# Kernel optimization log

Measured on AMD Instinct MI355X. Metric: run time of the kernel, lower is better.

## Reference

```python
import jax, jax.numpy as jnp
import numpy as np

N = 100000   # nodes
E = 600000   # edges
G = 64       # graphs in batch
H = 128      # hidden size
F_NODE = 2
F_EDGE = 7
RH = 500     # reghead size
NEG_SLOPE = 0.01
BN_EPS = 1e-5


def leaky(x):
    return jnp.where(x >= 0, x, NEG_SLOPE * x)


def gine_conv(x, src, dst, edge_attr, edge_W, edge_b, W1, b1, gamma, beta, W2, b2):
    # PyG GINEConv: message = ReLU(x_j + Lin(edge_attr)); sum-aggregate at dst;
    # out = nn((1+eps)*x + aggr) with eps=0; nn = Lin -> BN(train) -> LeakyReLU -> Lin -> LeakyReLU
    e = edge_attr @ edge_W.T + edge_b                 # [E, d_in]
    m = jax.nn.relu(x[src] + e)                       # gather + add + relu
    aggr = jax.ops.segment_sum(m, dst, num_segments=N)
    h = x + aggr
    h = h @ W1.T + b1                                 # [N, H]
    mu = jnp.mean(h, axis=0)
    var = jnp.var(h, axis=0)                          # biased, matches BN training
    h = gamma * (h - mu) * jax.lax.rsqrt(var + BN_EPS) + beta
    h = leaky(h)
    h = h @ W2.T + b2
    return leaky(h)


def setup_inputs() -> dict:
    key = jax.random.key(0)
    ks = jax.random.split(key, 24)

    def lin(k, out_d, in_d):
        s = 1.0 / np.sqrt(in_d)
        k1, k2 = jax.random.split(k)
        return (jax.random.uniform(k1, (out_d, in_d), jnp.float32, -s, s),
                jax.random.uniform(k2, (out_d,), jnp.float32, -s, s))

    x = jax.random.normal(ks[0], (N, F_NODE), jnp.float32)
    edge_index = jax.random.randint(ks[1], (2, E), 0, N, jnp.int32)
    batch = jnp.sort(jax.random.randint(ks[2], (N,), 0, G, jnp.int32))
    edge_attr = jax.random.normal(ks[3], (E, F_EDGE), jnp.float32)

    # layer 0 (in_dim = F_NODE)
    ew0, eb0 = lin(ks[4], F_NODE, F_EDGE)
    w10, b10 = lin(ks[5], H, F_NODE)
    g0, be0 = jnp.ones((H,), jnp.float32), jnp.zeros((H,), jnp.float32)
    w20, b20 = lin(ks[6], H, H)

    # 3 hidden layers, stacked (in_dim = H)
    L = 3
    ewS = jnp.stack([lin(ks[7 + i], H, F_EDGE)[0] for i in range(L)])
    ebS = jnp.stack([lin(jax.random.fold_in(ks[7 + i], 1), H, F_EDGE)[1] for i in range(L)])
    w1S = jnp.stack([lin(ks[10 + i], H, H)[0] for i in range(L)])
    b1S = jnp.stack([lin(jax.random.fold_in(ks[10 + i], 1), H, H)[1] for i in range(L)])
    gS = jnp.ones((L, H), jnp.float32)
    beS = jnp.zeros((L, H), jnp.float32)
    w2S = jnp.stack([lin(ks[13 + i], H, H)[0] for i in range(L)])
    b2S = jnp.stack([lin(jax.random.fold_in(ks[13 + i], 1), H, H)[1] for i in range(L)])

    wr, br = lin(ks[16], RH, H)
    we, be_ = lin(ks[17], 1, RH)

    return {"x": x, "edge_index": edge_index, "batch": batch, "edge_attr": edge_attr,
            "ew0": ew0, "eb0": eb0, "w10": w10, "b10": b10, "g0": g0, "be0": be0,
            "w20": w20, "b20": b20,
            "ewS": ewS, "ebS": ebS, "w1S": w1S, "b1S": b1S, "gS": gS, "beS": beS,
            "w2S": w2S, "b2S": b2S, "wr": wr, "br": br, "we": we, "be_": be_}


def reference(x, edge_index, batch, edge_attr,
              ew0, eb0, w10, b10, g0, be0, w20, b20,
              ewS, ebS, w1S, b1S, gS, beS, w2S, b2S,
              wr, br, we, be_):
    src, dst = edge_index[0], edge_index[1]
    h = gine_conv(x, src, dst, edge_attr, ew0, eb0, w10, b10, g0, be0, w20, b20)
    h = leaky(h)  # outer self.relu; dropout p=0 is identity
    for i in range(ewS.shape[0]):
        h = gine_conv(h, src, dst, edge_attr, ewS[i], ebS[i], w1S[i], b1S[i],
                      gS[i], beS[i], w2S[i], b2S[i])
        h = leaky(h)
    # global_mean_pool
    sums = jax.ops.segment_sum(h, batch, num_segments=G)
    cnt = jax.ops.segment_sum(jnp.ones((h.shape[0],), h.dtype), batch, num_segments=G)
    pooled = sums / jnp.maximum(cnt, 1.0)[:, None]
    # reghead_layers == 2
    r = leaky(pooled @ wr.T + br)
    return r @ we.T + be_
```

## Files before the change

kernel.cpp:

```cpp
#include <hip/hip_runtime.h>

#define NNODES 100000
#define NEDGES 600000
#define NGRAPH 64
#define HID 128
#define RHD 500
#define NB ((NNODES + 255) / 256)
#define EB ((NEDGES + 255) / 256)
#define GG ((NNODES + 63) / 64)

typedef __attribute__((ext_vector_type(8))) short short8;
typedef __attribute__((ext_vector_type(4))) float f32x4;

__device__ __forceinline__ float leaky1(float x) { return x >= 0.0f ? x : 0.01f * x; }

__device__ __forceinline__ void splitf(float a, unsigned short& h, unsigned short& l)
{
    unsigned u = __float_as_uint(a);
    unsigned r = (u + 0x7FFFu + ((u >> 16) & 1u)) & 0xFFFF0000u;
    h = (unsigned short)(r >> 16);
    float res = a - __uint_as_float(r);
    unsigned u2 = __float_as_uint(res);
    l = (unsigned short)((u2 + 0x7FFFu + ((u2 >> 16) & 1u)) >> 16);
}

__global__ __launch_bounds__(256) void hist_kernel(
    const int* __restrict__ ei, int* __restrict__ deg)
{
    int e = blockIdx.x * 256 + threadIdx.x;
    if (e < NEDGES) atomicAdd(&deg[ei[NEDGES + e]], 1);
}

__global__ __launch_bounds__(256) void scan_blk(
    const int* __restrict__ deg, int* __restrict__ incl, int* __restrict__ bsum)
{
    __shared__ int s[256];
    int t = threadIdx.x;
    int n = blockIdx.x * 256 + t;
    int v = (n < NNODES) ? deg[n] : 0;
    int x = v;
    s[t] = x;
    __syncthreads();
    for (int off = 1; off < 256; off <<= 1) {
        int y = (t >= off) ? s[t - off] : 0;
        __syncthreads();
        x += y; s[t] = x;
        __syncthreads();
    }
    if (n < NNODES) incl[n] = x;
    if (t == 255) bsum[blockIdx.x] = x;
}

__global__ __launch_bounds__(512) void scan_bsum(int* __restrict__ bsum, int nblk)
{
    __shared__ int s[512];
    int t = threadIdx.x;
    int v = (t < nblk) ? bsum[t] : 0;
    int x = v;
    s[t] = x;
    __syncthreads();
    for (int off = 1; off < 512; off <<= 1) {
        int y = (t >= off) ? s[t - off] : 0;
        __syncthreads();
        x += y; s[t] = x;
        __syncthreads();
    }
    if (t < nblk) bsum[t] = x - v;
}

__global__ __launch_bounds__(256) void finalize_rp(
    const int* __restrict__ deg, const int* __restrict__ bsum,
    int* __restrict__ rp, int* __restrict__ cursor)
{
    int n = blockIdx.x * 256 + threadIdx.x;
    if (n >= NNODES) return;
    int ig = rp[n] + bsum[blockIdx.x];
    int st = ig - deg[n];
    rp[n] = st;
    cursor[n] = st;
    if (n == NNODES - 1) rp[NNODES] = ig;
}

__global__ __launch_bounds__(256) void scatter_kernel(
    const int* __restrict__ ei, int* __restrict__ cursor, int* __restrict__ eid)
{
    int e = blockIdx.x * 256 + threadIdx.x;
    if (e >= NEDGES) return;
    int d = ei[NEDGES + e];
    int pos = atomicAdd(&cursor[d], 1);
    eid[pos] = e;
}

__global__ __launch_bounds__(256) void seg_sort(
    const int* __restrict__ rp, int* __restrict__ eid)
{
    int n = blockIdx.x * 256 + threadIdx.x;
    if (n >= NNODES) return;
    int beg = rp[n], end = rp[n + 1];
    for (int i = beg + 1; i < end; ++i) {
        int key = eid[i];
        int j = i - 1;
        while (j >= beg && eid[j] > key) { eid[j + 1] = eid[j]; --j; }
        eid[j + 1] = key;
    }
}

__global__ __launch_bounds__(256) void permute_kernel(
    const int* __restrict__ eid, const int* __restrict__ ei,
    const float* __restrict__ ea, int* __restrict__ srcp, float* __restrict__ eap)
{
    int p = blockIdx.x * 256 + threadIdx.x;
    if (p >= NEDGES) return;
    int id = eid[p];
    srcp[p] = ei[id];
    const float* s = ea + (size_t)id * 7;
    float* d = eap + (size_t)p * 7;
#pragma unroll
    for (int k = 0; k < 7; ++k) d[k] = s[k];
}

__global__ __launch_bounds__(256) void wsplit_all(
    const float* __restrict__ w20, const float* __restrict__ w1S,
    const float* __restrict__ w2S,
    unsigned short* __restrict__ wh, unsigned short* __restrict__ wl)
{
    int i = blockIdx.x * 256 + threadIdx.x;
    int m = i >> 14;
    int off = i & 16383;
    const float* src;
    if (m == 0) src = w20;
    else if (m <= 3) src = w1S + (size_t)(m - 1) * 16384;
    else src = w2S + (size_t)(m - 4) * 16384;
    unsigned short h, l;
    splitf(src[off], h, l);
    wh[i] = h;
    wl[i] = l;
}

__global__ __launch_bounds__(256) void aggregate0_kernel(
    const float* __restrict__ x, const int* __restrict__ rp,
    const int* __restrict__ srcp, const float* __restrict__ eap,
    const float* __restrict__ ew, const float* __restrict__ eb,
    float* __restrict__ aggr2)
{
    int n = blockIdx.x * 256 + threadIdx.x;
    if (n >= NNODES) return;
    float w0[7], w1[7];
#pragma unroll
    for (int k = 0; k < 7; ++k) { w0[k] = ew[k]; w1[k] = ew[7 + k]; }
    float e0b = eb[0], e1b = eb[1];
    float a0 = x[n * 2 + 0], a1 = x[n * 2 + 1];
    int beg = rp[n], end = rp[n + 1];
    for (int e = beg; e < end; ++e) {
        int s = srcp[e];
        const float* ap = eap + (size_t)e * 7;
        float t0 = e0b, t1 = e1b;
#pragma unroll
        for (int k = 0; k < 7; ++k) {
            float av = ap[k];
            t0 = fmaf(av, w0[k], t0);
            t1 = fmaf(av, w1[k], t1);
        }
        a0 += fmaxf(x[s * 2 + 0] + t0, 0.0f);
        a1 += fmaxf(x[s * 2 + 1] + t1, 0.0f);
    }
    aggr2[n * 2 + 0] = a0;
    aggr2[n * 2 + 1] = a1;
}

__global__ __launch_bounds__(256) void aggregate_kernel(
    const float* __restrict__ hin, const int* __restrict__ rp,
    const int* __restrict__ srcp, const float* __restrict__ eap,
    const float* __restrict__ ew, const float* __restrict__ eb,
    unsigned short* __restrict__ Ahi, unsigned short* __restrict__ Alo)
{
    int lane = threadIdx.x & 63;
    int w = threadIdx.x >> 6;
    int nbase = blockIdx.x * 32 + w * 8;
    float ew0[7], ew1[7];
#pragma unroll
    for (int k = 0; k < 7; ++k) {
        ew0[k] = ew[lane * 7 + k];
        ew1[k] = ew[(lane + 64) * 7 + k];
    }
    float eb0v = eb[lane], eb1v = eb[lane + 64];
    for (int n = nbase; n < nbase + 8; ++n) {
        float a0 = hin[(size_t)n * HID + lane];
        float a1 = hin[(size_t)n * HID + 64 + lane];
        int beg = rp[n], end = rp[n + 1];
        int e = beg;
        for (; e + 4 <= end; e += 4) {
            int s0 = srcp[e], s1 = srcp[e + 1], s2 = srcp[e + 2], s3 = srcp[e + 3];
            const float* ap = eap + (size_t)e * 7;
            float x00 = hin[(size_t)s0 * HID + lane];
            float x01 = hin[(size_t)s0 * HID + 64 + lane];
            float x10 = hin[(size_t)s1 * HID + lane];
            float x11 = hin[(size_t)s1 * HID + 64 + lane];
            float x20 = hin[(size_t)s2 * HID + lane];
            float x21 = hin[(size_t)s2 * HID + 64 + lane];
            float x30 = hin[(size_t)s3 * HID + lane];
            float x31 = hin[(size_t)s3 * HID + 64 + lane];
            float t00 = eb0v, t01 = eb1v, t10 = eb0v, t11 = eb1v;
            float t20 = eb0v, t21 = eb1v, t30 = eb0v, t31 = eb1v;
#pragma unroll
            for (int k = 0; k < 7; ++k) {
                float av0 = ap[k], av1 = ap[7 + k], av2 = ap[14 + k], av3 = ap[21 + k];
                t00 = fmaf(av0, ew0[k], t00); t01 = fmaf(av0, ew1[k], t01);
                t10 = fmaf(av1, ew0[k], t10); t11 = fmaf(av1, ew1[k], t11);
                t20 = fmaf(av2, ew0[k], t20); t21 = fmaf(av2, ew1[k], t21);
                t30 = fmaf(av3, ew0[k], t30); t31 = fmaf(av3, ew1[k], t31);
            }
            a0 += fmaxf(x00 + t00, 0.0f);
            a1 += fmaxf(x01 + t01, 0.0f);
            a0 += fmaxf(x10 + t10, 0.0f);
            a1 += fmaxf(x11 + t11, 0.0f);
            a0 += fmaxf(x20 + t20, 0.0f);
            a1 += fmaxf(x21 + t21, 0.0f);
            a0 += fmaxf(x30 + t30, 0.0f);
            a1 += fmaxf(x31 + t31, 0.0f);
        }
        for (; e < end; ++e) {
            int s = srcp[e];
            const float* ap = eap + (size_t)e * 7;
            float t0 = eb0v, t1 = eb1v;
#pragma unroll
            for (int k = 0; k < 7; ++k) {
                float av = ap[k];
                t0 = fmaf(av, ew0[k], t0);
                t1 = fmaf(av, ew1[k], t1);
            }
            float x0 = hin[(size_t)s * HID + lane];
            float x1 = hin[(size_t)s * HID + 64 + lane];
            a0 += fmaxf(x0 + t0, 0.0f);
            a1 += fmaxf(x1 + t1, 0.0f);
        }
        unsigned short h0, l0, h1v, l1v;
        splitf(a0, h0, l0);
        splitf(a1, h1v, l1v);
        size_t rb = (size_t)n * HID;
        Ahi[rb + lane] = h0;
        Ahi[rb + 64 + lane] = h1v;
        Alo[rb + lane] = l0;
        Alo[rb + 64 + lane] = l1v;
    }
}

__global__ __launch_bounds__(256) void gemm1_l0_kernel(
    const float* __restrict__ aggr2,
    const float* __restrict__ w1, const float* __restrict__ b1,
    float* __restrict__ h1)
{
    int n = blockIdx.x * 256 + threadIdx.x;
    if (n >= NNODES) return;
    float x0 = aggr2[n * 2 + 0];
    float x1 = aggr2[n * 2 + 1];
    float4* out4 = (float4*)(h1 + (size_t)n * HID);
    for (int j = 0; j < HID; j += 4) {
        float4 o;
        o.x = fmaf(x1, w1[(j + 0) * 2 + 1], fmaf(x0, w1[(j + 0) * 2 + 0], b1[j + 0]));
        o.y = fmaf(x1, w1[(j + 1) * 2 + 1], fmaf(x0, w1[(j + 1) * 2 + 0], b1[j + 1]));
        o.z = fmaf(x1, w1[(j + 2) * 2 + 1], fmaf(x0, w1[(j + 2) * 2 + 0], b1[j + 2]));
        o.w = fmaf(x1, w1[(j + 3) * 2 + 1], fmaf(x0, w1[(j + 3) * 2 + 0], b1[j + 3]));
        out4[j >> 2] = o;
    }
}

__global__ __launch_bounds__(256) void bn_stats_part(
    const float* __restrict__ h1, float* __restrict__ part)
{
    __shared__ float ls[HID], lq[HID];
    int c = threadIdx.x & 127;
    int half = threadIdx.x >> 7;
    int base = blockIdx.x * 256;
    int end = base + 256; if (end > NNODES) end = NNODES;
    float s = 0.0f, q = 0.0f;
    for (int r = base + half; r < end; r += 2) {
        float v = h1[(size_t)r * HID + c];
        s += v;
        q = fmaf(v, v, q);
    }
    if (half) { ls[c] = s; lq[c] = q; }
    __syncthreads();
    if (!half) {
        s += ls[c]; q += lq[c];
        part[(size_t)blockIdx.x * 256 + c] = s;
        part[(size_t)blockIdx.x * 256 + 128 + c] = q;
    }
}

__global__ __launch_bounds__(64) void bn_finalize(
    const float* __restrict__ part, int nblk,
    const float* __restrict__ gamma, const float* __restrict__ beta,
    float* __restrict__ scsh)
{
    int c = blockIdx.x;
    int lane = threadIdx.x;
    float s = 0.0f, q = 0.0f;
    for (int i = lane; i < nblk; i += 64) {
        s += part[(size_t)i * 256 + c];
        q += part[(size_t)i * 256 + 128 + c];
    }
#pragma unroll
    for (int off = 32; off >= 1; off >>= 1) {
        s += __shfl_down(s, off);
        q += __shfl_down(q, off);
    }
    if (lane == 0) {
        const float invN = 1.0f / (float)NNODES;
        float mu = s * invN;
        float var = fmaf(-mu, mu, q * invN);
        float iv = rsqrtf(var + 1e-5f);
        float sc = gamma[c] * iv;
        scsh[c] = sc;
        scsh[HID + c] = beta[c] - mu * sc;
    }
}

__global__ __launch_bounds__(256) void gemm1_direct(
    const unsigned short* __restrict__ Ahi, const unsigned short* __restrict__ Alo,
    const unsigned short* __restrict__ wh, const unsigned short* __restrict__ wl,
    const float* __restrict__ b1, float* __restrict__ h1,
    float* __restrict__ part)
{
    __shared__ float red[1024];
    const int t = threadIdx.x;
    const int lane = t & 63;
    const int wv = t >> 6;
    const int cl = lane & 15, g = lane >> 4;
    const int mb = blockIdx.x * 64;
    const int colbase = wv * 32;

    const unsigned short* wb_h0 = wh + (size_t)(colbase + cl) * HID + g * 8;
    const unsigned short* wb_h1 = wb_h0 + 16 * HID;
    const unsigned short* wb_l0 = wl + (size_t)(colbase + cl) * HID + g * 8;
    const unsigned short* wb_l1 = wb_l0 + 16 * HID;

    int arow[4];
#pragma unroll
    for (int rt = 0; rt < 4; ++rt) {
        int r = mb + rt * 16 + cl;
        arow[rt] = r < NNODES ? r : NNODES - 1;
    }

    f32x4 acc[4][2];
#pragma unroll
    for (int rt = 0; rt < 4; ++rt) {
        acc[rt][0] = (f32x4){0.f, 0.f, 0.f, 0.f};
        acc[rt][1] = (f32x4){0.f, 0.f, 0.f, 0.f};
    }

#pragma unroll
    for (int ks = 0; ks < 4; ++ks) {
        short8 bh0 = *(const short8*)(wb_h0 + ks * 32);
        short8 bh1 = *(const short8*)(wb_h1 + ks * 32);
        short8 bl0 = *(const short8*)(wb_l0 + ks * 32);
        short8 bl1 = *(const short8*)(wb_l1 + ks * 32);
        int koff = ks * 32 + g * 8;
#pragma unroll
        for (int rt = 0; rt < 4; ++rt) {
            short8 ah = *(const short8*)(Ahi + (size_t)arow[rt] * HID + koff);
            short8 al = *(const short8*)(Alo + (size_t)arow[rt] * HID + koff);
            acc[rt][0] = __builtin_amdgcn_mfma_f32_16x16x32_bf16(ah, bh0, acc[rt][0], 0, 0, 0);
            acc[rt][1] = __builtin_amdgcn_mfma_f32_16x16x32_bf16(ah, bh1, acc[rt][1], 0, 0, 0);
            acc[rt][0] = __builtin_amdgcn_mfma_f32_16x16x32_bf16(al, bh0, acc[rt][0], 0, 0, 0);
            acc[rt][1] = __builtin_amdgcn_mfma_f32_16x16x32_bf16(al, bh1, acc[rt][1], 0, 0, 0);
            acc[rt][0] = __builtin_amdgcn_mfma_f32_16x16x32_bf16(ah, bl0, acc[rt][0], 0, 0, 0);
            acc[rt][1] = __builtin_amdgcn_mfma_f32_16x16x32_bf16(ah, bl1, acc[rt][1], 0, 0, 0);
        }
    }

    float bj0 = b1[colbase + cl];
    float bj1 = b1[colbase + 16 + cl];
    float s0 = 0.f, q0 = 0.f, s1 = 0.f, q1 = 0.f;
#pragma unroll
    for (int rt = 0; rt < 4; ++rt) {
        int rbase = mb + rt * 16 + g * 4;
#pragma unroll
        for (int r = 0; r < 4; ++r) {
            int grow = rbase + r;
            if (grow < NNODES) {
                float o0 = acc[rt][0][r] + bj0;
                float o1 = acc[rt][1][r] + bj1;
                h1[(size_t)grow * HID + colbase + cl] = o0;
                h1[(size_t)grow * HID + colbase + 16 + cl] = o1;
                s0 += o0; q0 = fmaf(o0, o0, q0);
                s1 += o1; q1 = fmaf(o1, o1, q1);
            }
        }
    }
    red[(colbase + cl) * 4 + g] = s0;
    red[(colbase + 16 + cl) * 4 + g] = s1;
    red[512 + (colbase + cl) * 4 + g] = q0;
    red[512 + (colbase + 16 + cl) * 4 + g] = q1;
    __syncthreads();
    {
        int stat = t >> 7, col = t & 127;
        const float* bp = red + stat * 512 + col * 4;
        part[(size_t)blockIdx.x * 256 + stat * 128 + col] = bp[0] + bp[1] + bp[2] + bp[3];
    }
}

template<int PRE, int POST>
__global__ __launch_bounds__(256) void gemm_mfma(
    const float* __restrict__ Ain, const float* __restrict__ scsh,
    const unsigned short* __restrict__ wh, const unsigned short* __restrict__ wl,
    const float* __restrict__ bias, float* __restrict__ Hout)
{
    __shared__ __align__(16) short lds[16384];
    const int t = threadIdx.x;
    const int mb = blockIdx.x * 64;

    const float4* sc4 = (const float4*)scsh;
    const float4* sh4 = (const float4*)(scsh + HID);

#pragma unroll
    for (int u = 0; u < 4; ++u) {
        int idx = u * 256 + t;
        int row = idx >> 4, sl = idx & 15;
        float4 v0 = make_float4(0.f, 0.f, 0.f, 0.f);
        float4 v1 = make_float4(0.f, 0.f, 0.f, 0.f);
        int gr = mb + row;
        if (gr < NNODES) {
            const float4* p = (const float4*)(Ain + (size_t)gr * HID + sl * 8);
            v0 = p[0]; v1 = p[1];
            if (PRE) {
                float4 c0 = sc4[sl * 2], c1 = sc4[sl * 2 + 1];
                float4 s0 = sh4[sl * 2], s1 = sh4[sl * 2 + 1];
                v0.x = leaky1(fmaf(v0.x, c0.x, s0.x));
                v0.y = leaky1(fmaf(v0.y, c0.y, s0.y));
                v0.z = leaky1(fmaf(v0.z, c0.z, s0.z));
                v0.w = leaky1(fmaf(v0.w, c0.w, s0.w));
                v1.x = leaky1(fmaf(v1.x, c1.x, s1.x));
                v1.y = leaky1(fmaf(v1.y, c1.y, s1.y));
                v1.z = leaky1(fmaf(v1.z, c1.z, s1.z));
                v1.w = leaky1(fmaf(v1.w, c1.w, s1.w));
            }
        }
        unsigned short h[8], l[8];
        splitf(v0.x, h[0], l[0]); splitf(v0.y, h[1], l[1]);
        splitf(v0.z, h[2], l[2]); splitf(v0.w, h[3], l[3]);
        splitf(v1.x, h[4], l[4]); splitf(v1.y, h[5], l[5]);
        splitf(v1.z, h[6], l[6]); splitf(v1.w, h[7], l[7]);
        short8 hv, lv;
#pragma unroll
        for (int e = 0; e < 8; ++e) { hv[e] = (short)h[e]; lv[e] = (short)l[e]; }
        int byt = row * 256 + ((sl ^ (row & 7)) << 4);
        *(short8*)((char*)lds + byt) = hv;
        *(short8*)((char*)lds + 16384 + byt) = lv;
    }
    __syncthreads();

    const int lane = t & 63;
    const int wv = t >> 6;
    const int cl = lane & 15, g = lane >> 4, x = lane & 7;
    const int colbase = wv * 32;

    int aoff[4];
#pragma unroll
    for (int ks = 0; ks < 4; ++ks)
        aoff[ks] = cl * 256 + (((ks * 4 + g) ^ x) << 4);

    const unsigned short* wb_h0 = wh + (size_t)(colbase + cl) * HID + g * 8;
    const unsigned short* wb_h1 = wb_h0 + 16 * HID;
    const unsigned short* wb_l0 = wl + (size_t)(colbase + cl) * HID + g * 8;
    const unsigned short* wb_l1 = wb_l0 + 16 * HID;

    f32x4 acc[4][2];
#pragma unroll
    for (int rt = 0; rt < 4; ++rt) {
        acc[rt][0] = (f32x4){0.f, 0.f, 0.f, 0.f};
        acc[rt][1] = (f32x4){0.f, 0.f, 0.f, 0.f};
    }

#pragma unroll
    for (int ks = 0; ks < 4; ++ks) {
        short8 bh0 = *(const short8*)(wb_h0 + ks * 32);
        short8 bh1 = *(const short8*)(wb_h1 + ks * 32);
        short8 bl0 = *(const short8*)(wb_l0 + ks * 32);
        short8 bl1 = *(const short8*)(wb_l1 + ks * 32);
#pragma unroll
        for (int rt = 0; rt < 4; ++rt) {
            short8 ah = *(const short8*)((const char*)lds + (rt * 4096) + aoff[ks]);
            short8 al = *(const short8*)((const char*)lds + (16384 + rt * 4096) + aoff[ks]);
            acc[rt][0] = __builtin_amdgcn_mfma_f32_16x16x32_bf16(ah, bh0, acc[rt][0], 0, 0, 0);
            acc[rt][1] = __builtin_amdgcn_mfma_f32_16x16x32_bf16(ah, bh1, acc[rt][1], 0, 0, 0);
            acc[rt][0] = __builtin_amdgcn_mfma_f32_16x16x32_bf16(al, bh0, acc[rt][0], 0, 0, 0);
            acc[rt][1] = __builtin_amdgcn_mfma_f32_16x16x32_bf16(al, bh1, acc[rt][1], 0, 0, 0);
            acc[rt][0] = __builtin_amdgcn_mfma_f32_16x16x32_bf16(ah, bl0, acc[rt][0], 0, 0, 0);
            acc[rt][1] = __builtin_amdgcn_mfma_f32_16x16x32_bf16(ah, bl1, acc[rt][1], 0, 0, 0);
        }
    }

    float bj0 = bias[colbase + cl];
    float bj1 = bias[colbase + 16 + cl];
#pragma unroll
    for (int rt = 0; rt < 4; ++rt) {
        int rbase = mb + rt * 16 + g * 4;
#pragma unroll
        for (int r = 0; r < 4; ++r) {
            int grow = rbase + r;
            if (grow < NNODES) {
                float o0 = acc[rt][0][r] + bj0;
                float o1 = acc[rt][1][r] + bj1;
                if (POST) { o0 = leaky1(leaky1(o0)); o1 = leaky1(leaky1(o1)); }
                Hout[(size_t)grow * HID + colbase + cl] = o0;
                Hout[(size_t)grow * HID + colbase + 16 + cl] = o1;
            }
        }
    }
}

__global__ __launch_bounds__(256) void pool_kernel(
    const float* __restrict__ h, const int* __restrict__ batch,
    float* __restrict__ sums, float* __restrict__ cnt)
{
    int c = threadIdx.x & 127;
    int half = threadIdx.x >> 7;
    int base = blockIdx.x * 128 + half * 64;
    if (base >= NNODES) return;
    int end = base + 64; if (end > NNODES) end = NNODES;
    int g = batch[base];
    float acc = 0.0f, k = 0.0f;
    for (int n = base; n < end; ++n) {
        int gn = batch[n];
        if (gn != g) {
            atomicAdd(&sums[g * HID + c], acc);
            if (c == 0) atomicAdd(&cnt[g], k);
            acc = 0.0f; k = 0.0f; g = gn;
        }
        acc += h[(size_t)n * HID + c];
        k += 1.0f;
    }
    atomicAdd(&sums[g * HID + c], acc);
    if (c == 0) atomicAdd(&cnt[g], k);
}

__global__ __launch_bounds__(512) void reghead_kernel(
    const float* __restrict__ sums, const float* __restrict__ cnt,
    const float* __restrict__ wr, const float* __restrict__ br,
    const float* __restrict__ we, const float* __restrict__ be,
    float* __restrict__ out)
{
    __shared__ float pool[8 * HID];
    __shared__ float red[8][8];
    int g0 = blockIdx.x * 8;
    for (int i = threadIdx.x; i < 8 * HID; i += 512) {
        int g = g0 + (i >> 7);
        float c = cnt[g]; c = fmaxf(c, 1.0f);
        pool[i] = sums[g * HID + (i & 127)] / c;
    }
    __syncthreads();
    int j = threadIdx.x;
    float p[8];
#pragma unroll
    for (int g = 0; g < 8; ++g) p[g] = 0.0f;
    if (j < RHD) {
        float accs[8];
        float bjv = br[j];
#pragma unroll
        for (int g = 0; g < 8; ++g) accs[g] = bjv;
        const float4* wr4 = (const float4*)(wr + (size_t)j * HID);
        const float4* pool4 = (const float4*)pool;
        for (int k = 0; k < 32; ++k) {
            float4 w = wr4[k];
#pragma unroll
            for (int g = 0; g < 8; ++g) {
                float4 pv = pool4[g * 32 + k];
                accs[g] = fmaf(w.x, pv.x, accs[g]);
                accs[g] = fmaf(w.y, pv.y, accs[g]);
                accs[g] = fmaf(w.z, pv.z, accs[g]);
                accs[g] = fmaf(w.w, pv.w, accs[g]);
            }
        }
        float wej = we[j];
#pragma unroll
        for (int g = 0; g < 8; ++g) p[g] = leaky1(accs[g]) * wej;
    }
    int lane = threadIdx.x & 63, wid = threadIdx.x >> 6;
#pragma unroll
    for (int g = 0; g < 8; ++g) {
        float v = p[g];
        v += __shfl_down(v, 32); v += __shfl_down(v, 16); v += __shfl_down(v, 8);
        v += __shfl_down(v, 4);  v += __shfl_down(v, 2);  v += __shfl_down(v, 1);
        if (lane == 0) red[g][wid] = v;
    }
    __syncthreads();
    if (threadIdx.x < 8) {
        float sv = be[0];
#pragma unroll
        for (int w = 0; w < 8; ++w) sv += red[threadIdx.x][w];
        out[g0 + threadIdx.x] = sv;
    }
}

extern "C" void kernel_launch(void* const* d_in, const int* in_sizes, int n_in,
                              void* d_out, int out_size, void* d_ws, size_t ws_size,
                              hipStream_t stream)
{
    const float* x     = (const float*)d_in[0];
    const int*   ei    = (const int*)d_in[1];
    const int*   batch = (const int*)d_in[2];
    const float* ea    = (const float*)d_in[3];
    const float* ew0   = (const float*)d_in[4];
    const float* eb0   = (const float*)d_in[5];
    const float* w10   = (const float*)d_in[6];
    const float* b10   = (const float*)d_in[7];
    const float* g0v   = (const float*)d_in[8];
    const float* be0   = (const float*)d_in[9];
    const float* w20   = (const float*)d_in[10];
    const float* b20   = (const float*)d_in[11];
    const float* ewS   = (const float*)d_in[12];
    const float* ebS   = (const float*)d_in[13];
    const float* w1S   = (const float*)d_in[14];
    const float* b1S   = (const float*)d_in[15];
    const float* gS    = (const float*)d_in[16];
    const float* beS   = (const float*)d_in[17];
    const float* w2S   = (const float*)d_in[18];
    const float* b2S   = (const float*)d_in[19];
    const float* wr    = (const float*)d_in[20];
    const float* br    = (const float*)d_in[21];
    const float* we    = (const float*)d_in[22];
    const float* be_   = (const float*)d_in[23];

    float* ws    = (float*)d_ws;
    float* buf0  = ws;
    float* buf1  = buf0 + (size_t)NNODES * HID;
    float* buf2  = buf1 + (size_t)NNODES * HID;
    unsigned short* Ahi = (unsigned short*)buf2;
    unsigned short* Alo = Ahi + (size_t)NNODES * HID;
    float* part  = buf2 + (size_t)NNODES * HID;
    float* scsh  = part + (size_t)GG * 256;
    float* sums  = scsh + 256;
    float* cnt   = sums + NGRAPH * HID;
    float* aggr2 = cnt + NGRAPH;
    float* eap   = aggr2 + (size_t)NNODES * 2;
    int*   deg    = (int*)(eap + (size_t)NEDGES * 7);
    int*   cursor = deg + NNODES;
    int*   bsum   = cursor + NNODES;
    int*   rp     = bsum + 512;
    int*   eid    = rp + NNODES + 1;
    int*   srcp   = eid + NEDGES;
    unsigned short* whA = (unsigned short*)(srcp + NEDGES);
    unsigned short* wlA = whA + 7 * 16384;
    float* out   = (float*)d_out;

    hipMemsetAsync(deg, 0, (size_t)NNODES * sizeof(int), stream);
    hist_kernel<<<EB, 256, 0, stream>>>(ei, deg);
    scan_blk<<<NB, 256, 0, stream>>>(deg, rp, bsum);
    scan_bsum<<<1, 512, 0, stream>>>(bsum, NB);
    finalize_rp<<<NB, 256, 0, stream>>>(deg, bsum, rp, cursor);
    scatter_kernel<<<EB, 256, 0, stream>>>(ei, cursor, eid);
    seg_sort<<<NB, 256, 0, stream>>>(rp, eid);
    permute_kernel<<<EB, 256, 0, stream>>>(eid, ei, ea, srcp, eap);

    wsplit_all<<<448, 256, 0, stream>>>(w20, w1S, w2S, whA, wlA);

    aggregate0_kernel<<<NB, 256, 0, stream>>>(x, rp, srcp, eap, ew0, eb0, aggr2);
    gemm1_l0_kernel<<<NB, 256, 0, stream>>>(aggr2, w10, b10, buf0);
    bn_stats_part<<<NB, 256, 0, stream>>>(buf0, part);
    bn_finalize<<<HID, 64, 0, stream>>>(part, NB, g0v, be0, scsh);
    gemm_mfma<1, 1><<<GG, 256, 0, stream>>>(buf0, scsh, whA, wlA, b20, buf1);

    for (int i = 0; i < 3; ++i) {
        aggregate_kernel<<<NNODES / 32, 256, 0, stream>>>(buf1, rp, srcp, eap,
            ewS + (size_t)i * HID * 7, ebS + (size_t)i * HID, Ahi, Alo);
        gemm1_direct<<<GG, 256, 0, stream>>>(Ahi, Alo,
            whA + (size_t)(1 + i) * 16384, wlA + (size_t)(1 + i) * 16384,
            b1S + (size_t)i * HID, buf0, part);
        bn_finalize<<<HID, 64, 0, stream>>>(part, GG,
            gS + (size_t)i * HID, beS + (size_t)i * HID, scsh);
        gemm_mfma<1, 1><<<GG, 256, 0, stream>>>(buf0, scsh,
            whA + (size_t)(4 + i) * 16384, wlA + (size_t)(4 + i) * 16384,
            b2S + (size_t)i * HID, buf1);
    }

    hipMemsetAsync(sums, 0, (size_t)(NGRAPH * HID + NGRAPH) * sizeof(float), stream);
    pool_kernel<<<(NNODES + 127) / 128, 256, 0, stream>>>(buf1, batch, sums, cnt);
    reghead_kernel<<<NGRAPH / 8, 512, 0, stream>>>(sums, cnt, wr, br, we, be_, out);
}
```

Baseline: 724.9 us.

## Vectorize aggregate gathers, stage GEMM1 A tile in swizzled LDS, widen BN finalize

The aggregate kernel now gives each lane two adjacent channels. Neighbor rows are gathered with float2 loads, and the bf16 hi/lo split is written as packed 32-bit stores, which cuts the number of memory instructions per edge. The first GEMM now copies the 64-row A tile (hi and lo) into XOR-swizzled shared memory once. The MFMA loop then reads A from shared memory instead of issuing repeated global loads, and the statistics reduction reuses that buffer after a barrier. bn_finalize uses 256 threads with a shared-memory tree reduction, so each column's partials are reduced with more parallelism. Costs are more LDS use per block and extra barriers.

```diff
diff --git a/kernel.cpp b/kernel.cpp
--- a/kernel.cpp
+++ b/kernel.cpp
@@ -177,29 +177,26 @@
     int lane = threadIdx.x & 63;
     int w = threadIdx.x >> 6;
     int nbase = blockIdx.x * 32 + w * 8;
+    const int c0 = 2 * lane, c1 = 2 * lane + 1;
     float ew0[7], ew1[7];
 #pragma unroll
     for (int k = 0; k < 7; ++k) {
-        ew0[k] = ew[lane * 7 + k];
-        ew1[k] = ew[(lane + 64) * 7 + k];
-    }
-    float eb0v = eb[lane], eb1v = eb[lane + 64];
+        ew0[k] = ew[c0 * 7 + k];
+        ew1[k] = ew[c1 * 7 + k];
+    }
+    float eb0v = eb[c0], eb1v = eb[c1];
     for (int n = nbase; n < nbase + 8; ++n) {
-        float a0 = hin[(size_t)n * HID + lane];
-        float a1 = hin[(size_t)n * HID + 64 + lane];
+        float2 av = ((const float2*)(hin + (size_t)n * HID))[lane];
+        float a0 = av.x, a1 = av.y;
         int beg = rp[n], end = rp[n + 1];
         int e = beg;
         for (; e + 4 <= end; e += 4) {
             int s0 = srcp[e], s1 = srcp[e + 1], s2 = srcp[e + 2], s3 = srcp[e + 3];
             const float* ap = eap + (size_t)e * 7;
-            float x00 = hin[(size_t)s0 * HID + lane];
-            float x01 = hin[(size_t)s0 * HID + 64 + lane];
-            float x10 = hin[(size_t)s1 * HID + lane];
-            float x11 = hin[(size_t)s1 * HID + 64 + lane];
-            float x20 = hin[(size_t)s2 * HID + lane];
-            float x21 = hin[(size_t)s2 * HID + 64 + lane];
-            float x30 = hin[(size_t)s3 * HID + lane];
-            float x31 = hin[(size_t)s3 * HID + 64 + lane];
+            float2 x0 = ((const float2*)(hin + (size_t)s0 * HID))[lane];
+            float2 x1 = ((const float2*)(hin + (size_t)s1 * HID))[lane];
+            float2 x2 = ((const float2*)(hin + (size_t)s2 * HID))[lane];
+            float2 x3 = ((const float2*)(hin + (size_t)s3 * HID))[lane];
             float t00 = eb0v, t01 = eb1v, t10 = eb0v, t11 = eb1v;
             float t20 = eb0v, t21 = eb1v, t30 = eb0v, t31 = eb1v;
 #pragma unroll
@@ -210,18 +207,19 @@
                 t20 = fmaf(av2, ew0[k], t20); t21 = fmaf(av2, ew1[k], t21);
                 t30 = fmaf(av3, ew0[k], t30); t31 = fmaf(av3, ew1[k], t31);
             }
-            a0 += fmaxf(x00 + t00, 0.0f);
-            a1 += fmaxf(x01 + t01, 0.0f);
-            a0 += fmaxf(x10 + t10, 0.0f);
-            a1 += fmaxf(x11 + t11, 0.0f);
-            a0 += fmaxf(x20 + t20, 0.0f);
-            a1 += fmaxf(x21 + t21, 0.0f);
-            a0 += fmaxf(x30 + t30, 0.0f);
-            a1 += fmaxf(x31 + t31, 0.0f);
+            a0 += fmaxf(x0.x + t00, 0.0f);
+            a1 += fmaxf(x0.y + t01, 0.0f);
+            a0 += fmaxf(x1.x + t10, 0.0f);
+            a1 += fmaxf(x1.y + t11, 0.0f);
+            a0 += fmaxf(x2.x + t20, 0.0f);
+            a1 += fmaxf(x2.y + t21, 0.0f);
+            a0 += fmaxf(x3.x + t30, 0.0f);
+            a1 += fmaxf(x3.y + t31, 0.0f);
         }
         for (; e < end; ++e) {
             int s = srcp[e];
             const float* ap = eap + (size_t)e * 7;
+            float2 xv = ((const float2*)(hin + (size_t)s * HID))[lane];
             float t0 = eb0v, t1 = eb1v;
 #pragma unroll
             for (int k = 0; k < 7; ++k) {
@@ -229,19 +227,15 @@
                 t0 = fmaf(av, ew0[k], t0);
                 t1 = fmaf(av, ew1[k], t1);
             }
-            float x0 = hin[(size_t)s * HID + lane];
-            float x1 = hin[(size_t)s * HID + 64 + lane];
-            a0 += fmaxf(x0 + t0, 0.0f);
-            a1 += fmaxf(x1 + t1, 0.0f);
+            a0 += fmaxf(xv.x + t0, 0.0f);
+            a1 += fmaxf(xv.y + t1, 0.0f);
         }
         unsigned short h0, l0, h1v, l1v;
         splitf(a0, h0, l0);
         splitf(a1, h1v, l1v);
         size_t rb = (size_t)n * HID;
-        Ahi[rb + lane] = h0;
-        Ahi[rb + 64 + lane] = h1v;
-        Alo[rb + lane] = l0;
-        Alo[rb + 64 + lane] = l1v;
+        ((unsigned*)(Ahi + rb))[lane] = (unsigned)h0 | ((unsigned)h1v << 16);
+        ((unsigned*)(Alo + rb))[lane] = (unsigned)l0 | ((unsigned)l1v << 16);
     }
 }
 
@@ -288,27 +282,30 @@
     }
 }
 
-__global__ __launch_bounds__(64) void bn_finalize(
+__global__ __launch_bounds__(256) void bn_finalize(
     const float* __restrict__ part, int nblk,
     const float* __restrict__ gamma, const float* __restrict__ beta,
     float* __restrict__ scsh)
 {
+    __shared__ float ls[256], lq[256];
     int c = blockIdx.x;
-    int lane = threadIdx.x;
+    int t = threadIdx.x;
     float s = 0.0f, q = 0.0f;
-    for (int i = lane; i < nblk; i += 64) {
+    for (int i = t; i < nblk; i += 256) {
         s += part[(size_t)i * 256 + c];
         q += part[(size_t)i * 256 + 128 + c];
     }
-#pragma unroll
-    for (int off = 32; off >= 1; off >>= 1) {
-        s += __shfl_down(s, off);
-        q += __shfl_down(q, off);
-    }
-    if (lane == 0) {
+    ls[t] = s; lq[t] = q;
+    __syncthreads();
+#pragma unroll
+    for (int off = 128; off >= 1; off >>= 1) {
+        if (t < off) { ls[t] += ls[t + off]; lq[t] += lq[t + off]; }
+        __syncthreads();
+    }
+    if (t == 0) {
         const float invN = 1.0f / (float)NNODES;
-        float mu = s * invN;
-        float var = fmaf(-mu, mu, q * invN);
+        float mu = ls[0] * invN;
+        float var = fmaf(-mu, mu, lq[0] * invN);
         float iv = rsqrtf(var + 1e-5f);
         float sc = gamma[c] * iv;
         scsh[c] = sc;
@@ -316,31 +313,48 @@
     }
 }
 
-__global__ __launch_bounds__(256) void gemm1_direct(
+__global__ __launch_bounds__(256) void gemm1_lds(
     const unsigned short* __restrict__ Ahi, const unsigned short* __restrict__ Alo,
     const unsigned short* __restrict__ wh, const unsigned short* __restrict__ wl,
     const float* __restrict__ b1, float* __restrict__ h1,
     float* __restrict__ part)
 {
-    __shared__ float red[1024];
+    __shared__ __align__(16) short lds[16384];
     const int t = threadIdx.x;
+    const int mb = blockIdx.x * 64;
+
+#pragma unroll
+    for (int u = 0; u < 4; ++u) {
+        int idx = u * 256 + t;
+        int row = idx >> 4, sl = idx & 15;
+        int gr = mb + row;
+        short8 hv, lv;
+#pragma unroll
+        for (int e = 0; e < 8; ++e) { hv[e] = 0; lv[e] = 0; }
+        if (gr < NNODES) {
+            hv = *(const short8*)(Ahi + (size_t)gr * HID + sl * 8);
+            lv = *(const short8*)(Alo + (size_t)gr * HID + sl * 8);
+        }
+        int byt = row * 256 + ((sl ^ (row & 7)) << 4);
+        *(short8*)((char*)lds + byt) = hv;
+        *(short8*)((char*)lds + 16384 + byt) = lv;
+    }
+    __syncthreads();
+
     const int lane = t & 63;
     const int wv = t >> 6;
-    const int cl = lane & 15, g = lane >> 4;
-    const int mb = blockIdx.x * 64;
+    const int cl = lane & 15, g = lane >> 4, x = lane & 7;
     const int colbase = wv * 32;
+
+    int aoff[4];
+#pragma unroll
+    for (int ks = 0; ks < 4; ++ks)
+        aoff[ks] = cl * 256 + (((ks * 4 + g) ^ x) << 4);
 
     const unsigned short* wb_h0 = wh + (size_t)(colbase + cl) * HID + g * 8;
     const unsigned short* wb_h1 = wb_h0 + 16 * HID;
     const unsigned short* wb_l0 = wl + (size_t)(colbase + cl) * HID + g * 8;
     const unsigned short* wb_l1 = wb_l0 + 16 * HID;
-
-    int arow[4];
-#pragma unroll
-    for (int rt = 0; rt < 4; ++rt) {
-        int r = mb + rt * 16 + cl;
-        arow[rt] = r < NNODES ? r : NNODES - 1;
-    }
 
     f32x4 acc[4][2];
 #pragma unroll
@@ -355,11 +369,10 @@
         short8 bh1 = *(const short8*)(wb_h1 + ks * 32);
         short8 bl0 = *(const short8*)(wb_l0 + ks * 32);
         short8 bl1 = *(const short8*)(wb_l1 + ks * 32);
-        int koff = ks * 32 + g * 8;
 #pragma unroll
         for (int rt = 0; rt < 4; ++rt) {
-            short8 ah = *(const short8*)(Ahi + (size_t)arow[rt] * HID + koff);
-            short8 al = *(const short8*)(Alo + (size_t)arow[rt] * HID + koff);
+            short8 ah = *(const short8*)((const char*)lds + (rt * 4096) + aoff[ks]);
+            short8 al = *(const short8*)((const char*)lds + (16384 + rt * 4096) + aoff[ks]);
             acc[rt][0] = __builtin_amdgcn_mfma_f32_16x16x32_bf16(ah, bh0, acc[rt][0], 0, 0, 0);
             acc[rt][1] = __builtin_amdgcn_mfma_f32_16x16x32_bf16(ah, bh1, acc[rt][1], 0, 0, 0);
             acc[rt][0] = __builtin_amdgcn_mfma_f32_16x16x32_bf16(al, bh0, acc[rt][0], 0, 0, 0);
@@ -388,6 +401,8 @@
             }
         }
     }
+    __syncthreads();
+    float* red = (float*)lds;
     red[(colbase + cl) * 4 + g] = s0;
     red[(colbase + 16 + cl) * 4 + g] = s1;
     red[512 + (colbase + cl) * 4 + g] = q0;
@@ -658,16 +673,16 @@
     aggregate0_kernel<<<NB, 256, 0, stream>>>(x, rp, srcp, eap, ew0, eb0, aggr2);
     gemm1_l0_kernel<<<NB, 256, 0, stream>>>(aggr2, w10, b10, buf0);
     bn_stats_part<<<NB, 256, 0, stream>>>(buf0, part);
-    bn_finalize<<<HID, 64, 0, stream>>>(part, NB, g0v, be0, scsh);
+    bn_finalize<<<HID, 256, 0, stream>>>(part, NB, g0v, be0, scsh);
     gemm_mfma<1, 1><<<GG, 256, 0, stream>>>(buf0, scsh, whA, wlA, b20, buf1);
 
     for (int i = 0; i < 3; ++i) {
         aggregate_kernel<<<NNODES / 32, 256, 0, stream>>>(buf1, rp, srcp, eap,
             ewS + (size_t)i * HID * 7, ebS + (size_t)i * HID, Ahi, Alo);
-        gemm1_direct<<<GG, 256, 0, stream>>>(Ahi, Alo,
+        gemm1_lds<<<GG, 256, 0, stream>>>(Ahi, Alo,
             whA + (size_t)(1 + i) * 16384, wlA + (size_t)(1 + i) * 16384,
             b1S + (size_t)i * HID, buf0, part);
-        bn_finalize<<<HID, 64, 0, stream>>>(part, GG,
+        bn_finalize<<<HID, 256, 0, stream>>>(part, GG,
             gS + (size_t)i * HID, beS + (size_t)i * HID, scsh);
         gemm_mfma<1, 1><<<GG, 256, 0, stream>>>(buf0, scsh,
             whA + (size_t)(4 + i) * 16384, wlA + (size_t)(4 + i) * 16384,
```

Measured after the change: 688.2 us. -5.1%, faster.
